# Performance work log

Measured on AMD Instinct MI355X. Metric: run time of the kernel, lower is better.

The kernel has to match this reference:

```python
import jax, jax.numpy as jnp
import numpy as np
import math

B, T, C, E, H = 16, 256, 6, 512, 8


def setup_inputs() -> dict:
    key = jax.random.key(0)
    ks = jax.random.split(key, 5)
    std = 0.02
    return {
        "x": jax.random.normal(ks[0], (B, T, C, E), dtype=jnp.float32),
        "Wq": jax.random.normal(ks[1], (E, E), dtype=jnp.float32) * std,
        "bq": jnp.zeros((E,), dtype=jnp.float32),
        "Wk": jax.random.normal(ks[2], (E, E), dtype=jnp.float32) * std,
        "bk": jnp.zeros((E,), dtype=jnp.float32),
        "Wv": jax.random.normal(ks[3], (E, E), dtype=jnp.float32) * std,
        "bv": jnp.zeros((E,), dtype=jnp.float32),
        "Wp": jax.random.normal(ks[4], (E, E), dtype=jnp.float32) * std,
        "bp": jnp.zeros((E,), dtype=jnp.float32),
    }


def reference(x, Wq, bq, Wk, bk, Wv, bv, Wp, bp):
    b, t, c, e = x.shape
    hd = e // H
    # nn.Linear: y = x @ W^T + b, then view(B,T,C,H,hd).transpose(1,3) -> (B,H,C,T,hd)
    def heads(W, bias):
        y = jnp.einsum('btce,fe->btcf', x, W) + bias
        return y.reshape(b, t, c, H, hd).transpose(0, 3, 2, 1, 4)  # B,H,C,T,hd

    q = heads(Wq, bq)
    k = heads(Wk, bk)
    v = heads(Wv, bv)

    scale = 1.0 / math.sqrt(hd)
    att = jnp.einsum('bhctd,bhcsd->bhcts', q, k) * scale  # B,H,C,T,T
    causal = jnp.tril(jnp.ones((t, t), dtype=bool))
    att = jnp.where(causal, att, -jnp.inf)
    att = jax.nn.softmax(att, axis=-1)

    y = jnp.einsum('bhcts,bhcsd->bhctd', att, v)  # B,H,C,T,hd
    # permute(0,3,1,2,4) -> (B,T,H,C,hd), then view(B,T,C,E) (faithful to torch)
    y = y.transpose(0, 3, 1, 2, 4).reshape(b, t, c, e)
    return jnp.einsum('btce,fe->btcf', y, Wp) + bp
```

## Files before the change

kernel.cpp:

```cpp
#include <hip/hip_runtime.h>


typedef unsigned short u16;
typedef short bf16x8 __attribute__((ext_vector_type(8)));
typedef float f32x4 __attribute__((ext_vector_type(4)));
typedef u16 u16x4 __attribute__((ext_vector_type(4)));

#define MFMA16(a, b, c) __builtin_amdgcn_mfma_f32_16x16x32_bf16((a), (b), (c), 0, 0, 0)

__device__ __forceinline__ u16 f2b(float f) {
  union { float f; unsigned u; } v; v.f = f;
  unsigned r = v.u + 0x7fffu + ((v.u >> 16) & 1u);
  return (u16)(r >> 16);
}
__device__ __forceinline__ void gl_lds16(const void* g, void* l) {
  __builtin_amdgcn_global_load_lds(
      (const __attribute__((address_space(1))) void*)g,
      (__attribute__((address_space(3))) void*)l, 16, 0, 0);
}

__global__ void cvt_all(const float* __restrict__ x, u16* __restrict__ xdst,
                        const float* W0, const float* W1, const float* W2,
                        const float* W3, u16* __restrict__ wdst, int nxb) {
  const int bx = blockIdx.x;
  if (bx < nxb) {
    const size_t idx = ((size_t)bx * 256 + threadIdx.x) * 4;
    f32x4 v = *(const f32x4*)(x + idx);
    u16x4 o; o.x = f2b(v.x); o.y = f2b(v.y); o.z = f2b(v.z); o.w = f2b(v.w);
    *(u16x4*)(xdst + idx) = o;
  } else {
    const int wb = bx - nxb;
    const float* src = (wb < 256) ? W0 : (wb < 512) ? W1
                     : (wb < 768) ? W2 : W3;
    const int idx = ((wb & 255) * 256 + threadIdx.x) * 4;
    f32x4 v = *(const f32x4*)(src + idx);
    u16x4 o; o.x = f2b(v.x); o.y = f2b(v.y); o.z = f2b(v.z); o.w = f2b(v.w);
    *(u16x4*)(wdst + (size_t)(wb >> 8) * 262144 + idx) = o;
  }
}

#define STAGE(k, bi) do { \
  char* Sd_ = Sb + (bi) * 28672; \
  _Pragma("unroll") \
  for (int j_ = 0; j_ < 4; ++j_) \
    if (j_ < 3 || tid < 256) \
      gl_lds16(gsrc[j_] + (k) * 64, Sd_ + fl[j_]); \
} while (0)

__global__ __launch_bounds__(512, 2) void qkv_attn(
    const u16* __restrict__ xbf, const u16* __restrict__ wbf,
    const float* __restrict__ bq, const float* __restrict__ bk,
    const float* __restrict__ bv, u16* __restrict__ y_ws)
{
  const int blk = blockIdx.x;
  const int b   = blk / 48;
  const int h   = (blk / 6) % 8;
  const int c   = blk % 6;

  __shared__ u16 LDS[43008];
  char* Ksb  = (char*)LDS;
  char* Vtsb = (char*)LDS + 16384;
  char* Qsb  = (char*)LDS + 32768;
  char* Sb   = (char*)LDS;

  const int tid  = threadIdx.x;
  const int lane = tid & 63;
  const int wv   = tid >> 6;
  const int r    = lane & 15;
  const int qd   = lane >> 4;
  const int g    = wv >> 1;
  const int ch   = wv & 1;
  const int tiles[2] = { wv, 15 - wv };
  char* Pw = (char*)LDS + 65536 + wv * 2048;

  const char* gsrc[4]; int fl[4];
  #pragma unroll
  for (int j = 0; j < 4; ++j) {
    const int idx  = j * 512 + tid;
    const int flat = idx * 16;
    const int row  = flat >> 6;
    const int gc   = (((flat >> 4) & 3) - (row >> 1)) & 3;
    fl[j] = flat;
    if (row < 256) {
      gsrc[j] = (const char*)xbf +
                ((size_t)(b * 256 + row) * 6 + c) * 1024 + gc * 16;
    } else {
      const int sr  = row - 256;
      const int chw = sr / 96;
      const int rem = sr - chw * 96;
      const int tau = rem >> 5;
      const int nn  = rem & 31;
      gsrc[j] = (const char*)wbf + (size_t)tau * 524288 +
                (size_t)(h * 64 + chw * 32 + nn) * 1024 + gc * 16;
    }
  }

  int aoff[4], boff[3][2];
  #pragma unroll
  for (int mt = 0; mt < 4; ++mt) {
    const int row = g * 64 + mt * 16 + r;
    aoff[mt] = row * 64 + ((qd + (row >> 1)) & 3) * 16;
  }
  #pragma unroll
  for (int tau = 0; tau < 3; ++tau)
    #pragma unroll
    for (int nt = 0; nt < 2; ++nt) {
      const int row = 256 + ch * 96 + tau * 32 + nt * 16 + r;
      boff[tau][nt] = row * 64 + ((qd + (row >> 1)) & 3) * 16;
    }

  f32x4 acc[3][4][2] = {};

  STAGE(0, 0);
  STAGE(1, 1);

  #pragma unroll 2
  for (int kt = 0; kt < 16; ++kt) {
    if (kt < 15) { asm volatile("s_waitcnt vmcnt(3)\n\ts_barrier" ::: "memory"); }
    else         { asm volatile("s_waitcnt vmcnt(0)\n\ts_barrier" ::: "memory"); }

    if (kt + 2 < 16) STAGE(kt + 2, (kt + 2) % 3);

    char* Sc = Sb + (kt % 3) * 28672;
    bf16x8 af[4], bfr[3][2];
    #pragma unroll
    for (int mt = 0; mt < 4; ++mt)
      af[mt] = *(const bf16x8*)(Sc + aoff[mt]);
    #pragma unroll
    for (int tau = 0; tau < 3; ++tau)
      #pragma unroll
      for (int nt = 0; nt < 2; ++nt)
        bfr[tau][nt] = *(const bf16x8*)(Sc + boff[tau][nt]);

    #pragma unroll
    for (int tau = 0; tau < 3; ++tau)
      #pragma unroll
      for (int mt = 0; mt < 4; ++mt)
        #pragma unroll
        for (int nt = 0; nt < 2; ++nt)
          acc[tau][mt][nt] = MFMA16(af[mt], bfr[tau][nt], acc[tau][mt][nt]);
  }
  __syncthreads();

  float bqv[2], bkv[2], bvv[2];
  #pragma unroll
  for (int nt = 0; nt < 2; ++nt) {
    const int col = h * 64 + ch * 32 + nt * 16 + r;
    bqv[nt] = bq[col]; bkv[nt] = bk[col]; bvv[nt] = bv[col];
  }

  const int lo0 = ( qd      ^ (r & 7)) << 4;
  const int lo1 = ((4 + qd) ^ (r & 7)) << 4;

  #pragma unroll
  for (int mt = 0; mt < 4; ++mt)
    #pragma unroll
    for (int nt = 0; nt < 2; ++nt)
      #pragma unroll
      for (int rr = 0; rr < 4; ++rr) {
        const int t   = g * 64 + mt * 16 + qd * 4 + rr;
        const int col = ch * 32 + nt * 16 + r;
        const int qb  = t * 128 + (((col >> 3) ^ (t & 7)) << 4) + (r & 7) * 2;
        *(u16*)(Qsb + qb) = f2b(acc[0][mt][nt][rr] + bqv[nt]);
      }

  f32x4 o_acc[2][4] = {};
  float l_acc[2][4] = {{0.f,0.f,0.f,0.f},{0.f,0.f,0.f,0.f}};

  #pragma unroll
  for (int sc = 0; sc < 2; ++sc) {
    if (sc) __syncthreads();

    if ((g >> 1) == sc) {
      #pragma unroll
      for (int mt = 0; mt < 4; ++mt) {
        const int tl0 = g * 64 + mt * 16 + qd * 4 - sc * 128;
        #pragma unroll
        for (int nt = 0; nt < 2; ++nt) {
          u16x4 pv;
          #pragma unroll
          for (int rr = 0; rr < 4; ++rr)
            ((u16*)&pv)[rr] = f2b(acc[2][mt][nt][rr] + bvv[nt]);
          const int d  = ch * 32 + nt * 16 + r;
          const int vb = d * 256 + (((tl0 >> 3) ^ (r & 7)) << 4) + (tl0 & 7) * 2;
          *(u16x4*)(Vtsb + vb) = pv;
        }
        #pragma unroll
        for (int nt = 0; nt < 2; ++nt)
          #pragma unroll
          for (int rr = 0; rr < 4; ++rr) {
            const int tl  = tl0 + rr;
            const int col = ch * 32 + nt * 16 + r;
            const int kb  = tl * 128 + (((col >> 3) ^ (tl & 7)) << 4) + (r & 7) * 2;
            *(u16*)(Ksb + kb) = f2b(acc[1][mt][nt][rr] + bkv[nt]);
          }
      }
    }
    __syncthreads();

    #pragma unroll
    for (int ti = 0; ti < 2; ++ti) {
      if (sc == 1 && ti == 0) continue;
      const int mt  = tiles[ti];
      const int i0  = mt * 16;
      const int nch = (mt >> 2) + 1;

      bf16x8 qf[2];
      qf[0] = *(const bf16x8*)(Qsb + (i0 + r) * 128 + lo0);
      qf[1] = *(const bf16x8*)(Qsb + (i0 + r) * 128 + lo1);

      #pragma unroll
      for (int jcl = 0; jcl < 2; ++jcl) {
        const int jcg = sc * 2 + jcl;
        if (jcg >= nch) continue;
        const int j0l = jcl * 64;
        const int j0g = jcg * 64;

        f32x4 s[4] = {};
        #pragma unroll
        for (int nt = 0; nt < 4; ++nt) {
          const int krow = j0l + nt * 16 + r;
          bf16x8 kf0 = *(const bf16x8*)(Ksb + krow * 128 + lo0);
          s[nt] = MFMA16(qf[0], kf0, s[nt]);
          bf16x8 kf1 = *(const bf16x8*)(Ksb + krow * 128 + lo1);
          s[nt] = MFMA16(qf[1], kf1, s[nt]);
        }

        #pragma unroll
        for (int nt = 0; nt < 4; ++nt)
          #pragma unroll
          for (int rr = 0; rr < 4; ++rr) {
            const int i = i0 + qd * 4 + rr;
            const int j = j0g + nt * 16 + r;
            float p = __builtin_exp2f(fminf(s[nt][rr], 500.f) *
                                      0.1803368801111244f);
            if (j > i) p = 0.f;
            l_acc[ti][rr] += p;
            const int prow = qd * 4 + rr;
            const int pb = prow * 128 +
                (((nt * 2 + (r >> 3)) ^ (prow & 7)) << 4) + (r & 7) * 2;
            *(u16*)(Pw + pb) = f2b(p);
          }
        asm volatile("s_waitcnt lgkmcnt(0)" ::: "memory");

        bf16x8 pf[2];
        pf[0] = *(const bf16x8*)(Pw + r * 128 + lo0);
        pf[1] = *(const bf16x8*)(Pw + r * 128 + lo1);
        #pragma unroll
        for (int ntd = 0; ntd < 4; ++ntd) {
          const int vrow = ntd * 16 + r;
          bf16x8 vf0 = *(const bf16x8*)(Vtsb + vrow * 256 +
              ((((j0l >> 3) + qd) ^ (r & 7)) << 4));
          o_acc[ti][ntd] = MFMA16(pf[0], vf0, o_acc[ti][ntd]);
          bf16x8 vf1 = *(const bf16x8*)(Vtsb + vrow * 256 +
              ((((j0l >> 3) + 4 + qd) ^ (r & 7)) << 4));
          o_acc[ti][ntd] = MFMA16(pf[1], vf1, o_acc[ti][ntd]);
        }
      }
    }
  }

  const size_t obase = ((size_t)b * 256) * 3072 + h * 384 + c * 64;
  #pragma unroll
  for (int ti = 0; ti < 2; ++ti) {
    const int i0 = tiles[ti] * 16;
    float linv[4];
    #pragma unroll
    for (int rr = 0; rr < 4; ++rr) {
      float sum = l_acc[ti][rr];
      sum += __shfl_xor(sum, 1, 16);
      sum += __shfl_xor(sum, 2, 16);
      sum += __shfl_xor(sum, 4, 16);
      sum += __shfl_xor(sum, 8, 16);
      linv[rr] = 1.f / sum;
    }
    #pragma unroll
    for (int ntd = 0; ntd < 4; ++ntd)
      #pragma unroll
      for (int rr = 0; rr < 4; ++rr) {
        const int t = i0 + qd * 4 + rr;
        const int d = ntd * 16 + r;
        y_ws[obase + (size_t)t * 3072 + d] = f2b(o_acc[ti][ntd][rr] * linv[rr]);
      }
  }
}

__global__ __launch_bounds__(256, 3) void gemm_bt(
    const u16* __restrict__ A,
    const u16* W0, const u16* W1, const u16* W2,
    const float* bs0, const float* bs1, const float* bs2,
    u16* O0, u16* O1, u16* O2,
    float* OF,
    int qkv_mode)
{
  const int z = blockIdx.z;
  const u16* W    = (z == 0) ? W0 : (z == 1) ? W1 : W2;
  const float* bs = (z == 0) ? bs0 : (z == 1) ? bs1 : bs2;
  u16* O          = (z == 0) ? O0 : (z == 1) ? O1 : O2;

  const int m0 = blockIdx.x * 128;
  const int n0 = blockIdx.y * 128;

  __shared__ u16 As[128 * 32];
  __shared__ u16 Bs[128 * 32];

  const int tid  = threadIdx.x;
  const int lane = tid & 63;
  const int wv   = tid >> 6;
  const int r    = lane & 15;
  const int qd   = lane >> 4;
  const int wm   = (wv & 1) * 64;
  const int wn   = (wv >> 1) * 64;

  f32x4 acc[4][4] = {};

  for (int k0 = 0; k0 < 512; k0 += 32) {
    __syncthreads();
    #pragma unroll
    for (int it = 0; it < 2; ++it) {
      const int flat = (it * 256 + tid) * 16;
      const int row  = flat >> 6;
      const int swc  = (flat >> 4) & 3;
      const int gc   = (swc - (row >> 1)) & 3;
      gl_lds16((const char*)A + (size_t)(m0 + row) * 1024 + k0 * 2 + gc * 16,
               (char*)As + flat);
      gl_lds16((const char*)W + (size_t)(n0 + row) * 1024 + k0 * 2 + gc * 16,
               (char*)Bs + flat);
    }
    __syncthreads();

    bf16x8 af[4], bf[4];
    #pragma unroll
    for (int mt = 0; mt < 4; ++mt) {
      const int row = wm + mt * 16 + r;
      const int sw  = (qd + (row >> 1)) & 3;
      af[mt] = *(const bf16x8*)((const char*)As + row * 64 + sw * 16);
    }
    #pragma unroll
    for (int nt = 0; nt < 4; ++nt) {
      const int row = wn + nt * 16 + r;
      const int sw  = (qd + (row >> 1)) & 3;
      bf[nt] = *(const bf16x8*)((const char*)Bs + row * 64 + sw * 16);
    }
    #pragma unroll
    for (int mt = 0; mt < 4; ++mt)
      #pragma unroll
      for (int nt = 0; nt < 4; ++nt)
        acc[mt][nt] = MFMA16(af[mt], bf[nt], acc[mt][nt]);
  }

  float bv[4];
  #pragma unroll
  for (int nt = 0; nt < 4; ++nt) bv[nt] = bs[n0 + wn + nt * 16 + r];

  if (qkv_mode) {
    #pragma unroll
    for (int mt = 0; mt < 4; ++mt) {
      #pragma unroll
      for (int rr = 0; rr < 4; ++rr) {
        const int m   = m0 + wm + mt * 16 + qd * 4 + rr;
        const int b   = m / 1536;
        const int rem = m - b * 1536;
        const int t   = rem / 6;
        const int c   = rem - t * 6;
        #pragma unroll
        for (int nt = 0; nt < 4; ++nt) {
          const int f = n0 + wn + nt * 16 + r;
          const int hh = f >> 6;
          const int d = f & 63;
          const size_t addr = ((((size_t)b * 8 + hh) * 6 + c) * 256 + t) * 64 + d;
          O[addr] = f2b(acc[mt][nt][rr] + bv[nt]);
        }
      }
    }
  } else {
    #pragma unroll
    for (int mt = 0; mt < 4; ++mt) {
      #pragma unroll
      for (int rr = 0; rr < 4; ++rr) {
        const int m = m0 + wm + mt * 16 + qd * 4 + rr;
        #pragma unroll
        for (int nt = 0; nt < 4; ++nt) {
          const int f = n0 + wn + nt * 16 + r;
          OF[(size_t)m * 512 + f] = acc[mt][nt][rr] + bv[nt];
        }
      }
    }
  }
}

extern "C" void kernel_launch(void* const* d_in, const int* in_sizes, int n_in,
                              void* d_out, int out_size, void* d_ws, size_t ws_size,
                              hipStream_t stream) {
  const float* x  = (const float*)d_in[0];
  const float* Wq = (const float*)d_in[1];
  const float* bq = (const float*)d_in[2];
  const float* Wk = (const float*)d_in[3];
  const float* bk = (const float*)d_in[4];
  const float* Wv = (const float*)d_in[5];
  const float* bv = (const float*)d_in[6];
  const float* Wp = (const float*)d_in[7];
  const float* bp = (const float*)d_in[8];
  float* out = (float*)d_out;

  const size_t PER_B = 256 * 6 * 512;
  const size_t WSEG  = 4 * 262144;

  int NB = 16;
  while (NB > 1 && (WSEG + (size_t)2 * NB * PER_B) * 2 > ws_size) NB >>= 1;

  u16* wbf = (u16*)d_ws;
  u16* Wpb = wbf + 3 * 262144;

  const size_t slab = (size_t)NB * PER_B;
  u16* xbf  = wbf + WSEG;
  u16* y_ws = xbf + slab;

  const int nslab = 16 / NB;
  for (int s = 0; s < nslab; ++s) {
    const float* x_s  = x   + (size_t)s * NB * PER_B;
    float*      out_s = out + (size_t)s * NB * PER_B;
    const int nxb = NB * 768;
    const int grid = (s == 0) ? nxb + 1024 : nxb;
    cvt_all<<<dim3(grid), 256, 0, stream>>>(x_s, xbf, Wq, Wk, Wv, Wp, wbf, nxb);
    qkv_attn<<<dim3(NB * 48), 512, 0, stream>>>(xbf, wbf, bq, bk, bv, y_ws);
    gemm_bt<<<dim3(NB * 12, 4, 1), 256, 0, stream>>>(
        y_ws, Wpb, Wpb, Wpb, bp, bp, bp, nullptr, nullptr, nullptr, out_s, 0);
  }
}
```

Before: 202.7 us.

## Fuse fp32-to-bf16 conversion of x into QKV kernel staging

The separate conversion pass over x is removed. The attention kernel now loads fp32 x directly, converts it in registers and writes bf16 into LDS, while weights are still converted once by a small dedicated kernel. This drops a full write and re-read of the bf16 x copy in global memory and one launch, and it halves workspace use. In exchange the K-loop goes from a three-buffer async pipeline to a two-buffer one with a full vmcnt(0) wait and barrier every iteration, so load latency is exposed rather than overlapped with the MFMAs.

```diff
diff --git a/kernel.cpp b/kernel.cpp
--- a/kernel.cpp
+++ b/kernel.cpp
@@ -5,6 +5,7 @@
 typedef short bf16x8 __attribute__((ext_vector_type(8)));
 typedef float f32x4 __attribute__((ext_vector_type(4)));
 typedef u16 u16x4 __attribute__((ext_vector_type(4)));
+typedef u16 u16x8 __attribute__((ext_vector_type(8)));
 
 #define MFMA16(a, b, c) __builtin_amdgcn_mfma_f32_16x16x32_bf16((a), (b), (c), 0, 0, 0)
 
@@ -19,36 +20,41 @@
       (__attribute__((address_space(3))) void*)l, 16, 0, 0);
 }
 
-__global__ void cvt_all(const float* __restrict__ x, u16* __restrict__ xdst,
-                        const float* W0, const float* W1, const float* W2,
-                        const float* W3, u16* __restrict__ wdst, int nxb) {
-  const int bx = blockIdx.x;
-  if (bx < nxb) {
-    const size_t idx = ((size_t)bx * 256 + threadIdx.x) * 4;
-    f32x4 v = *(const f32x4*)(x + idx);
-    u16x4 o; o.x = f2b(v.x); o.y = f2b(v.y); o.z = f2b(v.z); o.w = f2b(v.w);
-    *(u16x4*)(xdst + idx) = o;
-  } else {
-    const int wb = bx - nxb;
-    const float* src = (wb < 256) ? W0 : (wb < 512) ? W1
-                     : (wb < 768) ? W2 : W3;
-    const int idx = ((wb & 255) * 256 + threadIdx.x) * 4;
-    f32x4 v = *(const f32x4*)(src + idx);
-    u16x4 o; o.x = f2b(v.x); o.y = f2b(v.y); o.z = f2b(v.z); o.w = f2b(v.w);
-    *(u16x4*)(wdst + (size_t)(wb >> 8) * 262144 + idx) = o;
-  }
-}
-
-#define STAGE(k, bi) do { \
-  char* Sd_ = Sb + (bi) * 28672; \
-  _Pragma("unroll") \
-  for (int j_ = 0; j_ < 4; ++j_) \
-    if (j_ < 3 || tid < 256) \
-      gl_lds16(gsrc[j_] + (k) * 64, Sd_ + fl[j_]); \
+__global__ void cvt_w(const float* W0, const float* W1, const float* W2,
+                      const float* W3, u16* dst) {
+  const float* src = (blockIdx.y == 0) ? W0 : (blockIdx.y == 1) ? W1
+                   : (blockIdx.y == 2) ? W2 : W3;
+  const int idx = (blockIdx.x * 256 + threadIdx.x) * 4;
+  f32x4 v = *(const f32x4*)(src + idx);
+  u16x4 o; o.x = f2b(v.x); o.y = f2b(v.y); o.z = f2b(v.z); o.w = f2b(v.w);
+  *(u16x4*)(dst + (size_t)blockIdx.y * 262144 + idx) = o;
+}
+
+#define STAGE_X(k, bi) do { \
+  const float* xs_ = xsrc + (k) * 32; \
+  f32x4 x0_ = *(const f32x4*)(xs_);      f32x4 x1_ = *(const f32x4*)(xs_ + 4); \
+  f32x4 x2_ = *(const f32x4*)(xs_ + 8);  f32x4 x3_ = *(const f32x4*)(xs_ + 12); \
+  u16x8 p0_, p1_; \
+  p0_[0]=f2b(x0_.x); p0_[1]=f2b(x0_.y); p0_[2]=f2b(x0_.z); p0_[3]=f2b(x0_.w); \
+  p0_[4]=f2b(x1_.x); p0_[5]=f2b(x1_.y); p0_[6]=f2b(x1_.z); p0_[7]=f2b(x1_.w); \
+  p1_[0]=f2b(x2_.x); p1_[1]=f2b(x2_.y); p1_[2]=f2b(x2_.z); p1_[3]=f2b(x2_.w); \
+  p1_[4]=f2b(x3_.x); p1_[5]=f2b(x3_.y); p1_[6]=f2b(x3_.z); p1_[7]=f2b(x3_.w); \
+  *(u16x8*)(Sb + (bi) * 28672 + xw0) = p0_; \
+  *(u16x8*)(Sb + (bi) * 28672 + xw1) = p1_; \
 } while (0)
 
+#define STAGE_W(k, bi) do { \
+  gl_lds16(wsrc[0] + (k) * 64, Sb + (bi) * 28672 + wfl[0]); \
+  if (tid < 256) gl_lds16(wsrc[1] + (k) * 64, Sb + (bi) * 28672 + wfl[1]); \
+} while (0)
+
+#define FENCE() do { \
+  asm volatile("s_waitcnt vmcnt(0) lgkmcnt(0)" ::: "memory"); \
+  __builtin_amdgcn_s_barrier(); \
+} while (0)
+
 __global__ __launch_bounds__(512, 2) void qkv_attn(
-    const u16* __restrict__ xbf, const u16* __restrict__ wbf,
+    const float* __restrict__ xf, const u16* __restrict__ wbf,
     const float* __restrict__ bq, const float* __restrict__ bk,
     const float* __restrict__ bv, u16* __restrict__ y_ws)
 {
@@ -57,7 +63,7 @@
   const int h   = (blk / 6) % 8;
   const int c   = blk % 6;
 
-  __shared__ u16 LDS[43008];
+  __shared__ u16 LDS[40960];
   char* Ksb  = (char*)LDS;
   char* Vtsb = (char*)LDS + 16384;
   char* Qsb  = (char*)LDS + 32768;
@@ -73,26 +79,27 @@
   const int tiles[2] = { wv, 15 - wv };
   char* Pw = (char*)LDS + 65536 + wv * 2048;
 
-  const char* gsrc[4]; int fl[4];
-  #pragma unroll
-  for (int j = 0; j < 4; ++j) {
+  const int xrow  = tid >> 1;
+  const int xhalf = tid & 1;
+  const float* xsrc = xf + ((size_t)(b * 256 + xrow) * 6 + c) * 512 + xhalf * 16;
+  const int xw0 = xrow * 64 + (((xhalf * 2    ) + (xrow >> 1)) & 3) * 16;
+  const int xw1 = xrow * 64 + (((xhalf * 2 + 1) + (xrow >> 1)) & 3) * 16;
+
+  const char* wsrc[2]; int wfl[2];
+  #pragma unroll
+  for (int j = 0; j < 2; ++j) {
     const int idx  = j * 512 + tid;
-    const int flat = idx * 16;
+    const int flat = 16384 + idx * 16;
     const int row  = flat >> 6;
     const int gc   = (((flat >> 4) & 3) - (row >> 1)) & 3;
-    fl[j] = flat;
-    if (row < 256) {
-      gsrc[j] = (const char*)xbf +
-                ((size_t)(b * 256 + row) * 6 + c) * 1024 + gc * 16;
-    } else {
-      const int sr  = row - 256;
-      const int chw = sr / 96;
-      const int rem = sr - chw * 96;
-      const int tau = rem >> 5;
-      const int nn  = rem & 31;
-      gsrc[j] = (const char*)wbf + (size_t)tau * 524288 +
-                (size_t)(h * 64 + chw * 32 + nn) * 1024 + gc * 16;
-    }
+    const int sr   = row - 256;
+    const int chw  = sr / 96;
+    const int rem  = sr - chw * 96;
+    const int tau  = rem >> 5;
+    const int nn   = rem & 31;
+    wfl[j]  = flat;
+    wsrc[j] = (const char*)wbf + (size_t)tau * 524288 +
+              (size_t)(h * 64 + chw * 32 + nn) * 1024 + gc * 16;
   }
 
   int aoff[4], boff[3][2];
@@ -111,17 +118,15 @@
 
   f32x4 acc[3][4][2] = {};
 
-  STAGE(0, 0);
-  STAGE(1, 1);
+  STAGE_X(0, 0); STAGE_W(0, 0);
+  FENCE();
 
   #pragma unroll 2
   for (int kt = 0; kt < 16; ++kt) {
-    if (kt < 15) { asm volatile("s_waitcnt vmcnt(3)\n\ts_barrier" ::: "memory"); }
-    else         { asm volatile("s_waitcnt vmcnt(0)\n\ts_barrier" ::: "memory"); }
-
-    if (kt + 2 < 16) STAGE(kt + 2, (kt + 2) % 3);
-
-    char* Sc = Sb + (kt % 3) * 28672;
+    const int cur = kt & 1;
+    if (kt < 15) { STAGE_X(kt + 1, cur ^ 1); STAGE_W(kt + 1, cur ^ 1); }
+
+    char* Sc = Sb + cur * 28672;
     bf16x8 af[4], bfr[3][2];
     #pragma unroll
     for (int mt = 0; mt < 4; ++mt)
@@ -139,6 +144,8 @@
         #pragma unroll
         for (int nt = 0; nt < 2; ++nt)
           acc[tau][mt][nt] = MFMA16(af[mt], bfr[tau][nt], acc[tau][mt][nt]);
+
+    if (kt < 15) FENCE();
   }
   __syncthreads();
 
@@ -407,23 +414,19 @@
   const size_t WSEG  = 4 * 262144;
 
   int NB = 16;
-  while (NB > 1 && (WSEG + (size_t)2 * NB * PER_B) * 2 > ws_size) NB >>= 1;
+  while (NB > 1 && (WSEG + (size_t)NB * PER_B) * 2 > ws_size) NB >>= 1;
 
   u16* wbf = (u16*)d_ws;
   u16* Wpb = wbf + 3 * 262144;
-
-  const size_t slab = (size_t)NB * PER_B;
-  u16* xbf  = wbf + WSEG;
-  u16* y_ws = xbf + slab;
+  u16* y_ws = wbf + WSEG;
+
+  cvt_w<<<dim3(256, 4), 256, 0, stream>>>(Wq, Wk, Wv, Wp, wbf);
 
   const int nslab = 16 / NB;
   for (int s = 0; s < nslab; ++s) {
     const float* x_s  = x   + (size_t)s * NB * PER_B;
     float*      out_s = out + (size_t)s * NB * PER_B;
-    const int nxb = NB * 768;
-    const int grid = (s == 0) ? nxb + 1024 : nxb;
-    cvt_all<<<dim3(grid), 256, 0, stream>>>(x_s, xbf, Wq, Wk, Wv, Wp, wbf, nxb);
-    qkv_attn<<<dim3(NB * 48), 512, 0, stream>>>(xbf, wbf, bq, bk, bv, y_ws);
+    qkv_attn<<<dim3(NB * 48), 512, 0, stream>>>(x_s, wbf, bq, bk, bv, y_ws);
     gemm_bt<<<dim3(NB * 12, 4, 1), 256, 0, stream>>>(
         y_ws, Wpb, Wpb, Wpb, bp, bp, bp, nullptr, nullptr, nullptr, out_s, 0);
   }
```

Result: slower. 221.8 us (+9.4%).
